# Kernel tuning notes

Hardware: AMD Instinct MI355X
Metric: run time of the kernel (lower is better)

Reference implementation:

```python
import jax, jax.numpy as jnp
import numpy as np

EPS = 1e-12  # matches torch F.normalize default eps

def setup_inputs() -> dict:
    key = jax.random.key(0)
    k1, k2, k3, k4 = jax.random.split(key, 4)
    B, C, H, W = 4, 256, 32, 32
    D, K = 2048, 16384
    return {
        "hidden_states": jax.random.normal(k1, (B, C, H, W), dtype=jnp.float32),
        "codebook": jax.random.normal(k2, (K, D), dtype=jnp.float32),
        "qc_w": jax.random.normal(k3, (D, C), dtype=jnp.float32) * 0.02,
        "qc_b": jax.random.normal(k4, (D,), dtype=jnp.float32) * 0.02,
    }

def _l2norm(x):
    # F.normalize(p=2, dim=-1): x / max(||x||, eps)
    n = jnp.sqrt(jnp.sum(x * x, axis=-1, keepdims=True))
    return x / jnp.maximum(n, EPS)

def reference(hidden_states, codebook, qc_w, qc_b):
    B, C, H, W = hidden_states.shape
    D = qc_w.shape[0]
    # quant_conv: 1x1 conv == per-pixel linear projection C -> D
    h = jnp.einsum("bchw,dc->bdhw", hidden_states, qc_w) + qc_b[None, :, None, None]
    # flatten to tokens: (B*H*W, D)
    flat = h.transpose(0, 2, 3, 1).reshape(-1, D)
    hn = _l2norm(flat)                  # (N, D)
    en = _l2norm(codebook)              # (K, D)
    sim = hn @ en.T                     # (N, K) cosine similarity
    idx = jnp.argmax(sim, axis=1)       # (N,)
    quant = en[idx]                     # gather normalized codes
    quant = quant.reshape(B, H, W, D).transpose(0, 3, 1, 2)
    return quant, idx
```

## Files before the change

### kernel.cpp

```cpp
#include <hip/hip_runtime.h>
#include <hip/hip_fp16.h>
#include <stdint.h>

#define NTOK 4096
#define KCB  16384
#define CAP  256
#define MAXL 8
#define MARGIN_C 0.02f
#define MARGIN_F 0.02f

typedef _Float16 f16;
typedef _Float16 f16x8 __attribute__((ext_vector_type(8)));
typedef float f32x4 __attribute__((ext_vector_type(4)));

typedef const __attribute__((address_space(1))) uint32_t* gptr_t;
typedef __attribute__((address_space(3))) uint32_t* lptr_t;
__device__ __forceinline__ void gload_lds16(const void* g, void* l) {
  __builtin_amdgcn_global_load_lds((gptr_t)g, (lptr_t)l, 16, 0, 0);
}

__global__ void k_init(int* cnt) {
  int i = blockIdx.x * 256 + threadIdx.x;
  if (i < NTOK) cnt[i] = 0;
}

__global__ __launch_bounds__(256) void k_build_wT(const float* qc_w, const float* qc_b, f16* wT) {
  __shared__ float tl[64][65];
  int d0 = blockIdx.x * 64, c0 = blockIdx.y * 64;
  int jj = threadIdx.x & 63, i0 = threadIdx.x >> 6;
  for (int ii = 0; ii < 64; ii += 4) {
    int i = ii + i0; int d = d0 + i; int c = c0 + jj;
    float v = 0.f;
    if (c < 256) v = qc_w[(size_t)d * 256 + c];
    else if (c == 256) v = qc_b[d];
    tl[i][jj] = v;
  }
  __syncthreads();
  for (int jj2 = 0; jj2 < 64; jj2 += 4) {
    int j = jj2 + i0; int i = threadIdx.x & 63;
    wT[(size_t)(c0 + j) * 2048 + d0 + i] = (f16)tl[i][j];
  }
}

__global__ __launch_bounds__(256) void k_build_x(const float* hid, f16* x16, float* x32) {
  __shared__ float tl[64][65];
  int hw0 = blockIdx.x * 64, c0 = blockIdx.y * 64, b = blockIdx.z;
  int jj = threadIdx.x & 63, i0 = threadIdx.x >> 6;
  for (int ii = 0; ii < 64; ii += 4) {
    int i = ii + i0;
    tl[i][jj] = hid[((size_t)b * 256 + c0 + i) * 1024 + hw0 + jj];
  }
  __syncthreads();
  for (int jj2 = 0; jj2 < 64; jj2 += 4) {
    int j = jj2 + i0; int i = threadIdx.x & 63;
    int t = b * 1024 + hw0 + j; float v = tl[i][j];
    x32[(size_t)t * 256 + c0 + i] = v;
    x16[(size_t)t * 320 + c0 + i] = (f16)v;
  }
  if (blockIdx.y == 0) {
    int tb = b * 1024 + hw0;
    for (int q = 0; q < 16; q++) {
      int idx2 = threadIdx.x * 16 + q;
      int tl2 = idx2 >> 6, p = idx2 & 63;
      x16[(size_t)(tb + tl2) * 320 + 256 + p] = (p == 0) ? (f16)1.0f : (f16)0.0f;
    }
  }
}

__global__ __launch_bounds__(256) void k_proj2b(const float* x32, const float* qc_w, const float* qc_b, double* h64) {
  __shared__ double At[16][128];
  __shared__ double Bt[16][16][9];
  int t0 = blockIdx.y * 128, d0 = blockIdx.x * 128;
  int tid = threadIdx.x;
  int tr = tid >> 4, dc = tid & 15;
  int srow = tid & 127, kh = (tid >> 7) * 8;
  int sg = srow >> 3, se = srow & 7;
  const float* pA = x32 + (size_t)(t0 + srow) * 256 + kh;
  const float* pB = qc_w + (size_t)(d0 + srow) * 256 + kh;
  f32x4 a0 = *(const f32x4*)pA, a1 = *(const f32x4*)(pA + 4);
  f32x4 b0 = *(const f32x4*)pB, b1 = *(const f32x4*)(pB + 4);
  double acc[8][8] = {};
  for (int kk = 0; kk < 256; kk += 16) {
    __syncthreads();
#pragma unroll
    for (int j = 0; j < 4; j++) {
      At[kh + j][srow] = (double)a0[j]; At[kh + 4 + j][srow] = (double)a1[j];
      Bt[kh + j][sg][se] = (double)b0[j]; Bt[kh + 4 + j][sg][se] = (double)b1[j];
    }
    __syncthreads();
    if (kk + 16 < 256) {
      a0 = *(const f32x4*)(pA + kk + 16); a1 = *(const f32x4*)(pA + kk + 20);
      b0 = *(const f32x4*)(pB + kk + 16); b1 = *(const f32x4*)(pB + kk + 20);
    }
#pragma unroll
    for (int k = 0; k < 16; k++) {
      double a[8], b[8];
#pragma unroll
      for (int j = 0; j < 8; j++) a[j] = At[k][tr * 8 + j];
#pragma unroll
      for (int j = 0; j < 8; j++) b[j] = Bt[k][dc][j];
#pragma unroll
      for (int i = 0; i < 8; i++)
#pragma unroll
        for (int j = 0; j < 8; j++)
          acc[i][j] = fma(a[i], b[j], acc[i][j]);
    }
  }
#pragma unroll
  for (int i = 0; i < 8; i++)
#pragma unroll
    for (int j = 0; j < 8; j++) {
      int col = d0 + dc * 8 + j;
      h64[(size_t)(t0 + tr * 8 + i) * 2048 + col] = acc[i][j] + (double)qc_b[col];
    }
}

__global__ __launch_bounds__(256) void k_pgemm4(const float* cb, const f16* wT, f16* P16kt,
                                                double* inv64, float* inv32) {
  __shared__ f16 Al[2][64][32];
  __shared__ f16 Bl[2][160][32];
  __shared__ double nsum[64][4];
  __shared__ double invsh[64];
  int j0 = blockIdx.x * 64;
  int c0 = blockIdx.y * 160;
  int tid = threadIdx.x, wid = tid >> 6, lane = tid & 63;
  int cl = lane & 15, g = lane >> 4;
  f32x4 acc[10];
#pragma unroll
  for (int n = 0; n < 10; n++) acc[n] = (f32x4)0.0f;
  int arow = tid & 63, aseg = tid >> 6;
  double s2 = 0.0;

  auto aload = [&](int kk, f32x4& v0, f32x4& v1) {
    v0 = *(const f32x4*)(cb + (size_t)(j0 + arow) * 2048 + kk + aseg * 8);
    v1 = *(const f32x4*)(cb + (size_t)(j0 + arow) * 2048 + kk + aseg * 8 + 4);
  };
  auto addnorm = [&](f32x4 v0, f32x4 v1) {
#pragma unroll
    for (int e = 0; e < 4; e++) {
      s2 += (double)v0[e] * (double)v0[e];
      s2 += (double)v1[e] * (double)v1[e];
    }
  };
  auto awrite = [&](int buf, f32x4 v0, f32x4 v1) {
    f16x8 h;
#pragma unroll
    for (int e = 0; e < 4; e++) { h[e] = (f16)v0[e]; h[4 + e] = (f16)v1[e]; }
    int sp = aseg ^ ((arow >> 1) & 3);
    *(f16x8*)((char*)&Al[buf][arow][0] + sp * 16) = h;
  };
  auto stageB = [&](int kk, int buf) {
#pragma unroll
    for (int i = 0; i < 3; i++) {
      int g2 = wid + 4 * i;
      if (g2 < 10) {
        int r0 = 16 * g2;
        int rl = r0 + (lane >> 2);
        int sl = (lane & 3) ^ ((rl >> 1) & 3);
        gload_lds16(wT + (size_t)(c0 + rl) * 2048 + kk + sl * 8, &Bl[buf][r0][0]);
      }
    }
  };
  auto rdA = [&](int buf, int r, int sg2) -> f16x8 {
    return *(const f16x8*)((const char*)&Al[buf][0][0] + r * 64 + ((sg2 ^ ((r >> 1) & 3)) << 4));
  };
  auto rdB = [&](int buf, int r, int sg2) -> f16x8 {
    return *(const f16x8*)((const char*)&Bl[buf][0][0] + r * 64 + ((sg2 ^ ((r >> 1) & 3)) << 4));
  };

  { f32x4 v0, v1; aload(0, v0, v1); addnorm(v0, v1); awrite(0, v0, v1); }
  stageB(0, 0);
  asm volatile("s_waitcnt vmcnt(0)" ::: "memory");
  __syncthreads();
  for (int s = 0; s < 64; s++) {
    int buf = s & 1;
    f32x4 v0, v1;
    if (s < 63) { aload((s + 1) * 32, v0, v1); stageB((s + 1) * 32, buf ^ 1); }
    f16x8 av = rdA(buf, 16 * wid + cl, g);
#pragma unroll
    for (int n = 0; n < 10; n++) {
      f16x8 bv = rdB(buf, 16 * n + cl, g);
      acc[n] = __builtin_amdgcn_mfma_f32_16x16x32_f16(av, bv, acc[n], 0, 0, 0);
    }
    if (s < 63) { addnorm(v0, v1); awrite(buf ^ 1, v0, v1); }
    asm volatile("s_waitcnt vmcnt(0)" ::: "memory");
    __syncthreads();
  }
  nsum[arow][aseg] = s2;
  __syncthreads();
  if (tid < 64) {
    double t = nsum[tid][0] + nsum[tid][1] + nsum[tid][2] + nsum[tid][3];
    double nn = sqrt(t); nn = fmax(nn, 1e-12);
    double iv = 1.0 / nn;
    invsh[tid] = iv;
    if (blockIdx.y == 0) { inv64[j0 + tid] = iv; inv32[j0 + tid] = (float)iv; }
  }
  __syncthreads();
#pragma unroll
  for (int r = 0; r < 4; r++) {
    int rloc = 16 * wid + 4 * g + r;
    int row = j0 + rloc;
    float sc = (float)invsh[rloc];
#pragma unroll
    for (int n = 0; n < 10; n++) {
      int c = c0 + 16 * n + cl;
      int ks = c >> 5;
      int sl = ((c & 31) >> 3) ^ ((row >> 1) & 3);
      P16kt[(((size_t)ks * KCB + row) << 5) + (sl << 3) + (c & 7)] = (f16)(acc[n][r] * sc);
    }
  }
}

__global__ __launch_bounds__(256) void k_screen10(const f16* x16, const f16* P16kt,
                                                  int* cnt, float* cand_v, int* cand_i) {
  __shared__ f16 Al[3][128][32];
  __shared__ f16 Bl[3][128][32];
  __shared__ float smx[128][2];
  int bid = blockIdx.x;
  int nb = ((bid & 7) << 4) | ((bid >> 3) & 15);
  int tb = bid >> 7;
  int n0 = nb * 128, t0 = tb * 128;
  int tid = threadIdx.x, wid = tid >> 6, lane = tid & 63;
  int wr = wid >> 1, wc = wid & 1;
  int cl = lane & 15, g = lane >> 4;
  f32x4 acc[4][4];
#pragma unroll
  for (int m = 0; m < 4; m++)
#pragma unroll
    for (int n = 0; n < 4; n++) acc[m][n] = (f32x4)0.0f;

  auto stageA = [&](int ks, int buf) {
#pragma unroll
    for (int i = 0; i < 2; i++) {
      int r0 = 32 * wid + 16 * i;
      int rl = r0 + (lane >> 2);
      int sl = (lane & 3) ^ ((rl >> 1) & 3);
      gload_lds16(x16 + (size_t)(t0 + rl) * 320 + ks * 32 + sl * 8, &Al[buf][r0][0]);
    }
  };
  auto stageB = [&](int ks, int buf) {
    const f16* src = P16kt + (((size_t)ks * KCB + n0) << 5) + wid * 1024 + lane * 8;
    gload_lds16(src, &Bl[buf][wid * 32][0]);
    gload_lds16(src + 512, &Bl[buf][wid * 32 + 16][0]);
  };
  auto rdA = [&](int buf, int r, int sg) -> f16x8 {
    return *(const f16x8*)((const char*)&Al[buf][0][0] + r * 64 + ((sg ^ ((r >> 1) & 3)) << 4));
  };
  auto rdB = [&](int buf, int r, int sg) -> f16x8 {
    return *(const f16x8*)((const char*)&Bl[buf][0][0] + r * 64 + ((sg ^ ((r >> 1) & 3)) << 4));
  };

  stageA(0, 0); stageB(0, 0);
  stageA(1, 1); stageB(1, 1);
#pragma unroll
  for (int s = 0; s < 10; s++) {
    const int buf = s % 3;
    if (s <= 8) asm volatile("s_waitcnt vmcnt(4)" ::: "memory");
    else        asm volatile("s_waitcnt vmcnt(0)" ::: "memory");
    __builtin_amdgcn_s_barrier();
    __builtin_amdgcn_sched_barrier(0);
    f16x8 av[4], bv[4];
#pragma unroll
    for (int m = 0; m < 4; m++) av[m] = rdA(buf, 64 * wr + 16 * m + cl, g);
#pragma unroll
    for (int n = 0; n < 4; n++) bv[n] = rdB(buf, 64 * wc + 16 * n + cl, g);
#pragma unroll
    for (int m = 0; m < 4; m++)
#pragma unroll
      for (int n = 0; n < 4; n++)
        acc[m][n] = __builtin_amdgcn_mfma_f32_16x16x32_f16(av[m], bv[n], acc[m][n], 0, 0, 0);
    if (s + 2 < 10) {
      const int nb2 = (s + 2) % 3;
      stageA(s + 2, nb2); stageB(s + 2, nb2);
    }
  }

#pragma unroll
  for (int m = 0; m < 4; m++) {
#pragma unroll
    for (int r = 0; r < 4; r++) {
      float v = -3.4e38f;
#pragma unroll
      for (int n = 0; n < 4; n++) v = fmaxf(v, acc[m][n][r]);
      v = fmaxf(v, __shfl_xor(v, 1));
      v = fmaxf(v, __shfl_xor(v, 2));
      v = fmaxf(v, __shfl_xor(v, 4));
      v = fmaxf(v, __shfl_xor(v, 8));
      if (cl == 0) smx[64 * wr + 16 * m + 4 * g + r][wc] = v;
    }
  }
  __syncthreads();

  uint32_t* lcnt = (uint32_t*)(&Al[0][0][0]);
  float*    lval = (float*)(lcnt + 128);
  int*      lidx = (int*)(lval + 128 * MAXL);
  if (tid < 128) lcnt[tid] = 0;
  __syncthreads();

#pragma unroll
  for (int m = 0; m < 4; m++) {
#pragma unroll
    for (int r = 0; r < 4; r++) {
      int rloc = 64 * wr + 16 * m + 4 * g + r;
      float lim = fmaxf(smx[rloc][0], smx[rloc][1]) - MARGIN_C;
#pragma unroll
      for (int n = 0; n < 4; n++) {
        float vv = acc[m][n][r];
        if (vv >= lim) {
          uint32_t p = atomicAdd(&lcnt[rloc], 1u);
          int code = n0 + 64 * wc + 16 * n + cl;
          if (p < MAXL) { lval[rloc * MAXL + p] = vv; lidx[rloc * MAXL + p] = code; }
          else {
            int slot = atomicAdd(&cnt[t0 + rloc], 1);
            if (slot < CAP) { cand_v[(t0 + rloc) * CAP + slot] = vv; cand_i[(t0 + rloc) * CAP + slot] = code; }
          }
        }
      }
    }
  }
  __syncthreads();

  if (tid < 128) {
    int lc = (int)lcnt[tid]; if (lc > MAXL) lc = MAXL;
    if (lc > 0) {
      int row = t0 + tid;
      int base = atomicAdd(&cnt[row], lc);
      for (int i = 0; i < lc; i++) {
        int slot = base + i;
        if (slot < CAP) {
          cand_v[row * CAP + slot] = lval[tid * MAXL + i];
          cand_i[row * CAP + slot] = lidx[tid * MAXL + i];
        }
      }
    }
  }
}

__global__ __launch_bounds__(256) void k_rescore2(const double* h64, const float* cb, const double* inv64,
                                                  const int* cnt, const float* cand_v, const int* cand_i,
                                                  float* idxf, int* idxi) {
  __shared__ double hsh[2048];
  __shared__ double red[256];
  __shared__ int redi[256];
  __shared__ float wmax[4];
  int t = blockIdx.x, tid = threadIdx.x;
  int lane = tid & 63, wid = tid >> 6;
  for (int i = 0; i < 8; i++) hsh[tid + 256 * i] = h64[(size_t)t * 2048 + tid + 256 * i];
  __syncthreads();
  int ctot = cnt[t];
  double bV = -1e300; int bI = 0x7fffffff;
  if (ctot <= CAP) {
    int n = ctot;
    float gm = -3.4e38f;
    for (int c = tid; c < n; c += 256) gm = fmaxf(gm, cand_v[t * CAP + c]);
    for (int o = 32; o; o >>= 1) gm = fmaxf(gm, __shfl_xor(gm, o));
    if (lane == 0) wmax[wid] = gm;
    __syncthreads();
    float gmax = fmaxf(fmaxf(wmax[0], wmax[1]), fmaxf(wmax[2], wmax[3]));
    float lim = gmax - MARGIN_F;
    for (int c = 0; c < n; c++) {
      float v = cand_v[t * CAP + c];
      if (v < lim) continue;
      int code = cand_i[t * CAP + c];
      const float* row = cb + (size_t)code * 2048;
      double p = 0.0;
      for (int i = 0; i < 8; i++) { int d = tid + 256 * i; p += hsh[d] * (double)row[d]; }
      red[tid] = p; __syncthreads();
      for (int s2 = 128; s2; s2 >>= 1) { if (tid < s2) red[tid] += red[tid + s2]; __syncthreads(); }
      if (tid == 0) {
        double sv = red[0] * inv64[code];
        if (sv > bV || (sv == bV && code < bI)) { bV = sv; bI = code; }
      }
      __syncthreads();
    }
  } else {
    for (int code = tid; code < KCB; code += 256) {
      const float* row = cb + (size_t)code * 2048;
      double p = 0.0;
      for (int d = 0; d < 2048; d++) p += hsh[d] * (double)row[d];
      double sv = p * inv64[code];
      if (sv > bV || (sv == bV && code < bI)) { bV = sv; bI = code; }
    }
    red[tid] = bV; redi[tid] = bI; __syncthreads();
    for (int s2 = 128; s2; s2 >>= 1) {
      if (tid < s2) {
        double ov = red[tid + s2]; int oi = redi[tid + s2];
        if (ov > red[tid] || (ov == red[tid] && oi < redi[tid])) { red[tid] = ov; redi[tid] = oi; }
      }
      __syncthreads();
    }
    if (tid == 0) { bV = red[0]; bI = redi[0]; }
  }
  if (tid == 0) { idxi[t] = bI; idxf[t] = (float)bI; }
}

__global__ __launch_bounds__(256) void k_quant(const float* cb, const float* inv32, const int* idxi, float* out0) {
  int hw = blockIdx.x * 256 + threadIdx.x;
  int d = blockIdx.y, b = blockIdx.z;
  int t = b * 1024 + hw;
  int row = idxi[t];
  out0[((size_t)b * 2048 + d) * 1024 + hw] = cb[(size_t)row * 2048 + d] * inv32[row];
}

extern "C" void kernel_launch(void* const* d_in, const int* in_sizes, int n_in,
                              void* d_out, int out_size, void* d_ws, size_t ws_size,
                              hipStream_t stream) {
  const float* hid = (const float*)d_in[0];
  const float* cb  = (const float*)d_in[1];
  const float* qw  = (const float*)d_in[2];
  const float* qb  = (const float*)d_in[3];
  float* out = (float*)d_out;

  char* w = (char*)d_ws;
  size_t off = 0;
  auto alloc = [&](size_t bytes) -> void* {
    void* p = w + off;
    off += (bytes + 255) & ~(size_t)255;
    return p;
  };
  double* h64   = (double*)alloc((size_t)NTOK * 2048 * 8);
  f16*    x16   = (f16*)   alloc((size_t)NTOK * 320 * 2);
  float*  x32   = (float*) alloc((size_t)NTOK * 256 * 4);
  f16*    wT    = (f16*)   alloc((size_t)320 * 2048 * 2);
  f16*    P16kt = (f16*)   alloc((size_t)10 * KCB * 32 * 2);
  double* inv64 = (double*)alloc((size_t)KCB * 8);
  float*  inv32 = (float*) alloc((size_t)KCB * 4);
  int*    cnt   = (int*)   alloc((size_t)NTOK * 4);
  float*  cand_v= (float*) alloc((size_t)NTOK * CAP * 4);
  int*    cand_i= (int*)   alloc((size_t)NTOK * CAP * 4);
  int*    idxi  = (int*)   alloc((size_t)NTOK * 4);

  k_init<<<16, 256, 0, stream>>>(cnt);
  k_build_wT<<<dim3(32, 5), 256, 0, stream>>>(qw, qb, wT);
  k_build_x<<<dim3(16, 4, 4), 256, 0, stream>>>(hid, x16, x32);
  k_proj2b<<<dim3(16, 32), 256, 0, stream>>>(x32, qw, qb, h64);
  k_pgemm4<<<dim3(256, 2), 256, 0, stream>>>(cb, wT, P16kt, inv64, inv32);
  k_screen10<<<4096, 256, 0, stream>>>(x16, P16kt, cnt, cand_v, cand_i);
  k_rescore2<<<NTOK, 256, 0, stream>>>(h64, cb, inv64, cnt, cand_v, cand_i, out + 8388608, idxi);
  k_quant<<<dim3(4, 2048, 4), 256, 0, stream>>>(cb, inv32, idxi, out);
}
```

Measured before the change: 401.3 us.

## Use FP64 MFMA for projection and single-wave rescoring per token

Replaces the scalar double-precision projection GEMM with an FP64 MFMA kernel. The MFMA kernel first probes the accumulator layout at runtime and sets a flag, so a fallback kernel runs the old path only if the layout check fails. The rescoring kernel drops from 256 to 64 threads per token and uses wave shuffles instead of shared-memory tree reductions and barriers, reading h64 straight from global memory. This removes LDS traffic and synchronisation, at the cost of an extra launch and a runtime layout probe.

```diff
diff --git a/kernel.cpp b/kernel.cpp
--- a/kernel.cpp
+++ b/kernel.cpp
@@ -12,6 +12,7 @@
 typedef _Float16 f16;
 typedef _Float16 f16x8 __attribute__((ext_vector_type(8)));
 typedef float f32x4 __attribute__((ext_vector_type(4)));
+typedef double f64x4 __attribute__((ext_vector_type(4)));
 
 typedef const __attribute__((address_space(1))) uint32_t* gptr_t;
 typedef __attribute__((address_space(3))) uint32_t* lptr_t;
@@ -19,9 +20,10 @@
   __builtin_amdgcn_global_load_lds((gptr_t)g, (lptr_t)l, 16, 0, 0);
 }
 
-__global__ void k_init(int* cnt) {
+__global__ void k_init(int* cnt, int* bad) {
   int i = blockIdx.x * 256 + threadIdx.x;
   if (i < NTOK) cnt[i] = 0;
+  if (blockIdx.x == 0 && threadIdx.x == 0) *bad = 0;
 }
 
 __global__ __launch_bounds__(256) void k_build_wT(const float* qc_w, const float* qc_b, f16* wT) {
@@ -67,7 +69,100 @@
   }
 }
 
-__global__ __launch_bounds__(256) void k_proj2b(const float* x32, const float* qc_w, const float* qc_b, double* h64) {
+__global__ __launch_bounds__(256) void k_proj_mfma(const float* x32, const float* qc_w, const float* qc_b,
+                                                   double* h64, int* bad) {
+  __shared__ double At[32][66];
+  __shared__ double Bt[32][130];
+  int d0 = blockIdx.x * 128, t0 = blockIdx.y * 64;
+  int tid = threadIdx.x, wid = tid >> 6, lane = tid & 63;
+  int cl = lane & 15, g = lane >> 4;
+
+  double ta1 = (double)cl;
+  double tb1 = (g == 0) ? 1.0 : 0.0;
+  f64x4 tc1 = {0.0, 0.0, 0.0, 0.0};
+  tc1 = __builtin_amdgcn_mfma_f64_16x16x4f64(ta1, tb1, tc1, 0, 0, 0);
+  double ta2 = (g == 0) ? 1.0 : 0.0;
+  double tb2 = (g == 0) ? (double)cl : 0.0;
+  f64x4 tc2 = {0.0, 0.0, 0.0, 0.0};
+  tc2 = __builtin_amdgcn_mfma_f64_16x16x4f64(ta2, tb2, tc2, 0, 0, 0);
+  bool std_ok = true, alt_ok = true, col_ok = true;
+#pragma unroll
+  for (int r = 0; r < 4; r++) {
+    std_ok = std_ok && (tc1[r] == (double)(4 * g + r));
+    alt_ok = alt_ok && (tc1[r] == (double)(g + 4 * r));
+    col_ok = col_ok && (tc2[r] == (double)cl);
+  }
+  unsigned long long mstd = __ballot(std_ok), malt = __ballot(alt_ok), mcol = __ballot(col_ok);
+  bool all_std = (mstd == ~0ull), all_alt = (malt == ~0ull), all_col = (mcol == ~0ull);
+  bool good = (all_std || all_alt) && all_col;
+  if (!good) { if (tid == 0) atomicOr(bad, 1); return; }
+  int use_alt = all_alt ? 1 : 0;
+
+  int t_a = tid & 63, ka = (tid >> 6) * 8;
+  int d_b = tid & 127, kb = (tid >> 7) * 16;
+  f32x4 ra0, ra1, rb0, rb1, rb2, rb3;
+  auto ldregs = [&](int kc) {
+    ra0 = *(const f32x4*)(x32 + (size_t)(t0 + t_a) * 256 + kc + ka);
+    ra1 = *(const f32x4*)(x32 + (size_t)(t0 + t_a) * 256 + kc + ka + 4);
+    rb0 = *(const f32x4*)(qc_w + (size_t)(d0 + d_b) * 256 + kc + kb);
+    rb1 = *(const f32x4*)(qc_w + (size_t)(d0 + d_b) * 256 + kc + kb + 4);
+    rb2 = *(const f32x4*)(qc_w + (size_t)(d0 + d_b) * 256 + kc + kb + 8);
+    rb3 = *(const f32x4*)(qc_w + (size_t)(d0 + d_b) * 256 + kc + kb + 12);
+  };
+  ldregs(0);
+
+  f64x4 acc[4][2];
+#pragma unroll
+  for (int i = 0; i < 4; i++)
+#pragma unroll
+    for (int j = 0; j < 2; j++) acc[i][j] = (f64x4)0.0;
+
+  for (int c = 0; c < 8; c++) {
+    __syncthreads();
+#pragma unroll
+    for (int e = 0; e < 4; e++) {
+      At[ka + e][t_a] = (double)ra0[e];
+      At[ka + 4 + e][t_a] = (double)ra1[e];
+      Bt[kb + e][d_b] = (double)rb0[e];
+      Bt[kb + 4 + e][d_b] = (double)rb1[e];
+      Bt[kb + 8 + e][d_b] = (double)rb2[e];
+      Bt[kb + 12 + e][d_b] = (double)rb3[e];
+    }
+    __syncthreads();
+    if (c < 7) ldregs((c + 1) * 32);
+#pragma unroll
+    for (int k4 = 0; k4 < 8; k4++) {
+      int k = k4 * 4 + g;
+      double a[4], b[2];
+#pragma unroll
+      for (int i = 0; i < 4; i++) a[i] = At[k][16 * i + cl];
+#pragma unroll
+      for (int j = 0; j < 2; j++) b[j] = Bt[k][32 * wid + 16 * j + cl];
+#pragma unroll
+      for (int i = 0; i < 4; i++)
+#pragma unroll
+        for (int j = 0; j < 2; j++)
+          acc[i][j] = __builtin_amdgcn_mfma_f64_16x16x4f64(a[i], b[j], acc[i][j], 0, 0, 0);
+    }
+  }
+#pragma unroll
+  for (int i = 0; i < 4; i++)
+#pragma unroll
+    for (int j = 0; j < 2; j++) {
+      int d = d0 + 32 * wid + 16 * j + cl;
+      double bias = (double)qc_b[d];
+#pragma unroll
+      for (int r = 0; r < 4; r++) {
+        int row = use_alt ? (g + 4 * r) : (4 * g + r);
+        int t = t0 + 16 * i + row;
+        h64[(size_t)t * 2048 + d] = acc[i][j][r] + bias;
+      }
+    }
+}
+
+__global__ __launch_bounds__(256) void k_proj_fb(const float* x32, const float* qc_w, const float* qc_b,
+                                                 double* h64, const int* bad) {
+  if (*bad == 0) return;
   __shared__ double At[16][128];
   __shared__ double Bt[16][16][9];
   int t0 = blockIdx.y * 128, d0 = blockIdx.x * 128;
@@ -336,62 +431,50 @@
   }
 }
 
-__global__ __launch_bounds__(256) void k_rescore2(const double* h64, const float* cb, const double* inv64,
-                                                  const int* cnt, const float* cand_v, const int* cand_i,
-                                                  float* idxf, int* idxi) {
-  __shared__ double hsh[2048];
-  __shared__ double red[256];
-  __shared__ int redi[256];
-  __shared__ float wmax[4];
-  int t = blockIdx.x, tid = threadIdx.x;
-  int lane = tid & 63, wid = tid >> 6;
-  for (int i = 0; i < 8; i++) hsh[tid + 256 * i] = h64[(size_t)t * 2048 + tid + 256 * i];
-  __syncthreads();
+__global__ __launch_bounds__(64) void k_rescore3(const double* h64, const float* cb, const double* inv64,
+                                                 const int* cnt, const float* cand_v, const int* cand_i,
+                                                 float* idxf, int* idxi) {
+  int t = blockIdx.x;
+  int lane = threadIdx.x;
   int ctot = cnt[t];
   double bV = -1e300; int bI = 0x7fffffff;
+  const double* hrow = h64 + (size_t)t * 2048;
   if (ctot <= CAP) {
-    int n = ctot;
     float gm = -3.4e38f;
-    for (int c = tid; c < n; c += 256) gm = fmaxf(gm, cand_v[t * CAP + c]);
+    for (int c = lane; c < ctot; c += 64) gm = fmaxf(gm, cand_v[t * CAP + c]);
+#pragma unroll
     for (int o = 32; o; o >>= 1) gm = fmaxf(gm, __shfl_xor(gm, o));
-    if (lane == 0) wmax[wid] = gm;
-    __syncthreads();
-    float gmax = fmaxf(fmaxf(wmax[0], wmax[1]), fmaxf(wmax[2], wmax[3]));
-    float lim = gmax - MARGIN_F;
-    for (int c = 0; c < n; c++) {
+    float lim = gm - MARGIN_F;
+    for (int c = 0; c < ctot; c++) {
       float v = cand_v[t * CAP + c];
       if (v < lim) continue;
       int code = cand_i[t * CAP + c];
-      const float* row = cb + (size_t)code * 2048;
+      const float* crow = cb + (size_t)code * 2048;
       double p = 0.0;
-      for (int i = 0; i < 8; i++) { int d = tid + 256 * i; p += hsh[d] * (double)row[d]; }
-      red[tid] = p; __syncthreads();
-      for (int s2 = 128; s2; s2 >>= 1) { if (tid < s2) red[tid] += red[tid + s2]; __syncthreads(); }
-      if (tid == 0) {
-        double sv = red[0] * inv64[code];
-        if (sv > bV || (sv == bV && code < bI)) { bV = sv; bI = code; }
+#pragma unroll
+      for (int e = 0; e < 32; e++) {
+        int d = lane + 64 * e;
+        p = fma(hrow[d], (double)crow[d], p);
       }
-      __syncthreads();
-    }
-  } else {
-    for (int code = tid; code < KCB; code += 256) {
-      const float* row = cb + (size_t)code * 2048;
-      double p = 0.0;
-      for (int d = 0; d < 2048; d++) p += hsh[d] * (double)row[d];
+#pragma unroll
+      for (int o = 32; o; o >>= 1) p += __shfl_xor(p, o);
       double sv = p * inv64[code];
       if (sv > bV || (sv == bV && code < bI)) { bV = sv; bI = code; }
     }
-    red[tid] = bV; redi[tid] = bI; __syncthreads();
-    for (int s2 = 128; s2; s2 >>= 1) {
-      if (tid < s2) {
-        double ov = red[tid + s2]; int oi = redi[tid + s2];
-        if (ov > red[tid] || (ov == red[tid] && oi < redi[tid])) { red[tid] = ov; redi[tid] = oi; }
+  } else {
+    for (int code = 0; code < KCB; code++) {
+      const float* crow = cb + (size_t)code * 2048;
+      double p = 0.0;
+      for (int e = 0; e < 32; e++) {
+        int d = lane + 64 * e;
+        p = fma(hrow[d], (double)crow[d], p);
       }
-      __syncthreads();
-    }
-    if (tid == 0) { bV = red[0]; bI = redi[0]; }
-  }
-  if (tid == 0) { idxi[t] = bI; idxf[t] = (float)bI; }
+      for (int o = 32; o; o >>= 1) p += __shfl_xor(p, o);
+      double sv = p * inv64[code];
+      if (sv > bV || (sv == bV && code < bI)) { bV = sv; bI = code; }
+    }
+  }
+  if (lane == 0) { idxi[t] = bI; idxf[t] = (float)bI; }
 }
 
 __global__ __launch_bounds__(256) void k_quant(const float* cb, const float* inv32, const int* idxi, float* out0) {
@@ -429,13 +512,15 @@
   float*  cand_v= (float*) alloc((size_t)NTOK * CAP * 4);
   int*    cand_i= (int*)   alloc((size_t)NTOK * CAP * 4);
   int*    idxi  = (int*)   alloc((size_t)NTOK * 4);
-
-  k_init<<<16, 256, 0, stream>>>(cnt);
+  int*    bad   = (int*)   alloc(256);
+
+  k_init<<<16, 256, 0, stream>>>(cnt, bad);
   k_build_wT<<<dim3(32, 5), 256, 0, stream>>>(qw, qb, wT);
   k_build_x<<<dim3(16, 4, 4), 256, 0, stream>>>(hid, x16, x32);
-  k_proj2b<<<dim3(16, 32), 256, 0, stream>>>(x32, qw, qb, h64);
+  k_proj_mfma<<<dim3(16, 64), 256, 0, stream>>>(x32, qw, qb, h64, bad);
+  k_proj_fb<<<dim3(16, 32), 256, 0, stream>>>(x32, qw, qb, h64, bad);
   k_pgemm4<<<dim3(256, 2), 256, 0, stream>>>(cb, wT, P16kt, inv64, inv32);
   k_screen10<<<4096, 256, 0, stream>>>(x16, P16kt, cnt, cand_v, cand_i);
-  k_rescore2<<<NTOK, 256, 0, stream>>>(h64, cb, inv64, cnt, cand_v, cand_i, out + 8388608, idxi);
+  k_rescore3<<<NTOK, 64, 0, stream>>>(h64, cb, inv64, cnt, cand_v, cand_i, out + 8388608, idxi);
   k_quant<<<dim3(4, 2048, 4), 256, 0, stream>>>(cb, inv32, idxi, out);
 }
```

New measurement: 383.8 us. 4.4% less time.
